# Optimization experiments

Measured on AMD Instinct MI355X. Metric: run time of the kernel, lower is better.

The kernel has to match this reference:

```python
import jax, jax.numpy as jnp
import numpy as np

N_NODES = 100000
N_EDGES = 800000
ANNOT = 92
HID = 64
N_STEPS = 8
N_IDX = 20000


def setup_inputs() -> dict:
    key = jax.random.key(0)
    ks = jax.random.split(key, 12)
    s = 1.0 / np.sqrt(HID)
    return {
        'x': jax.random.normal(ks[0], (N_NODES, ANNOT), dtype=jnp.float32),
        'edge_index': jax.random.randint(ks[1], (2, N_EDGES), 0, N_NODES, dtype=jnp.int64),
        'idx': jax.random.randint(ks[2], (N_IDX,), 0, N_NODES, dtype=jnp.int64),
        'W_red': jax.random.normal(ks[3], (ANNOT, HID), dtype=jnp.float32) / np.sqrt(ANNOT),
        'b_red': jnp.zeros((HID,), dtype=jnp.float32),
        'W_g': jax.random.normal(ks[4], (N_STEPS, HID, HID), dtype=jnp.float32) * s,
        'w_ih': jax.random.normal(ks[5], (3 * HID, HID), dtype=jnp.float32) * s,
        'w_hh': jax.random.normal(ks[6], (3 * HID, HID), dtype=jnp.float32) * s,
        'b_ih': jax.random.normal(ks[7], (3 * HID,), dtype=jnp.float32) * s,
        'b_hh': jax.random.normal(ks[8], (3 * HID,), dtype=jnp.float32) * s,
        'W_lin': jax.random.normal(ks[9], (HID, 1), dtype=jnp.float32) * s,
        'b_lin': jnp.zeros((1,), dtype=jnp.float32),
    }


def _gru_cell(a, h, w_ih, w_hh, b_ih, b_hh):
    # a: aggregated messages [N, H]; h: hidden state [N, H]
    gi = a @ w_ih.T + b_ih  # [N, 3H]
    gh = h @ w_hh.T + b_hh
    i_r, i_z, i_n = jnp.split(gi, 3, axis=-1)
    h_r, h_z, h_n = jnp.split(gh, 3, axis=-1)
    r = jax.nn.sigmoid(i_r + h_r)
    z = jax.nn.sigmoid(i_z + h_z)
    n = jnp.tanh(i_n + r * h_n)
    return (1.0 - z) * n + z * h


def reference(x, edge_index, idx, W_red, b_red, W_g, w_ih, w_hh, b_ih, b_hh, W_lin, b_lin):
    src, dst = edge_index[0], edge_index[1]
    h = x @ W_red + b_red  # [N, H]

    def step(h, Wt):
        m = h @ Wt                                  # [N, H] per-step transform
        msg = jnp.take(m, src, axis=0)              # gather along edges [E, H]
        aggr = jax.ops.segment_sum(msg, dst, num_segments=N_NODES)  # scatter-add
        h_new = _gru_cell(aggr, h, w_ih, w_hh, b_ih, b_hh)
        return h_new, None

    h, _ = jax.lax.scan(step, h, W_g)
    sel = jnp.take(h, idx, axis=0)                  # index_select [B, H]
    return jax.nn.sigmoid(sel @ W_lin + b_lin)      # [B, 1]
```

## Files before the change

### kernel.cpp

```cpp
#include <hip/hip_runtime.h>
#include <hip/hip_bf16.h>

#define NN 100000
#define HH 64
#define AN 92
#define NSTEP 8
#define NGRP 6250
#define RB 768
#define CAP 64

typedef float f4v __attribute__((ext_vector_type(4)));
typedef short s8v __attribute__((ext_vector_type(8)));

__device__ __forceinline__ float sigf(float x) { return 1.0f / (1.0f + __expf(-x)); }
__device__ __forceinline__ float tanhfast(float x) { return 1.0f - 2.0f / (1.0f + __expf(2.0f * x)); }

__device__ __forceinline__ unsigned short tobf(float x) {
    __hip_bfloat16 b = __float2bfloat16(x);
    return __builtin_bit_cast(unsigned short, b);
}
__device__ __forceinline__ float frombf(unsigned short u) {
    return __int_as_float(((unsigned)u) << 16);
}

__device__ __forceinline__ int packpos(int k, int r) {
    int T = r >> 4, kh = k >> 5;
    int lane = ((k >> 3) & 3) * 16 + (r & 15);
    int j = k & 7;
    return ((T * 2 + kh) * 64 + lane) * 8 + j;
}

__global__ __launch_bounds__(256) void k_wcp(const float* __restrict__ Wg,
                                             const float* __restrict__ w_ih,
                                             const float* __restrict__ w_hh,
                                             unsigned short* __restrict__ Wcp,
                                             unsigned short* __restrict__ Whp) {
    __shared__ float wl[192 * 65];
    int wb = blockIdx.x;
    if (wb < 384) {
        for (int i = threadIdx.x; i < 192 * 64; i += 256) {
            int r = i >> 6, q = i & 63;
            wl[r * 65 + q] = w_ih[i];
        }
        __syncthreads();
        int gid = wb * 256 + threadIdx.x;
        int r = gid % 192;
        int k = (gid / 192) & 63;
        int t = gid / (192 * 64);
        const float* wg = Wg + t * 4096 + k * 64;
        float acc = 0.f;
#pragma unroll
        for (int q = 0; q < 64; ++q) acc = fmaf(wg[q], wl[r * 65 + q], acc);
        Wcp[t * 12288 + packpos(k, r)] = tobf(acc);
    } else {
        int gid = (wb - 384) * 256 + threadIdx.x;
        if (gid >= 192 * 64) return;
        int r = gid >> 6, k = gid & 63;
        Whp[packpos(k, r)] = tobf(w_hh[r * 64 + k]);
    }
}

__global__ __launch_bounds__(256) void k_plred(const int* __restrict__ src,
                                               const int* __restrict__ dst,
                                               int* __restrict__ cnt,
                                               int* __restrict__ srt, int E,
                                               const float* __restrict__ x,
                                               const float* __restrict__ W,
                                               const float* __restrict__ b,
                                               unsigned short* __restrict__ hb) {
    __shared__ float xl[16][96];
    __shared__ float wl[96 * 64];
    int tid = threadIdx.x;
    if (blockIdx.x >= RB) {
        int e = (blockIdx.x - RB) * 256 + tid;
        if (e < E) {
            int d = dst[e];
            int pos = atomicAdd(cnt + d, 1);
            if (pos < CAP) srt[d * CAP + pos] = src[e];
        }
        return;
    }
    for (int i = tid; i < AN * 64; i += 256) wl[i] = W[i];
    wl[AN * 64 + tid] = 0.f;
    if (tid < 64) xl[tid >> 2][AN + (tid & 3)] = 0.f;
    int lane = tid & 63, wave = tid >> 6;
    float bj = b[lane];

    for (int g = blockIdx.x; g < NGRP; g += RB) {
        int n0 = g * 16;
        __syncthreads();
        for (int i = tid; i < 16 * AN; i += 256)
            xl[i / AN][i % AN] = x[(size_t)n0 * AN + i];
        __syncthreads();
        float a[4];
#pragma unroll
        for (int u = 0; u < 4; ++u) a[u] = bj;
#pragma unroll
        for (int k4 = 0; k4 < 96; k4 += 4) {
            float4 xv[4];
#pragma unroll
            for (int u = 0; u < 4; ++u) xv[u] = *(const float4*)&xl[wave * 4 + u][k4];
#pragma unroll
            for (int kk = 0; kk < 4; ++kk) {
                float wv = wl[(k4 + kk) * 64 + lane];
                a[0] = fmaf(((const float*)&xv[0])[kk], wv, a[0]);
                a[1] = fmaf(((const float*)&xv[1])[kk], wv, a[1]);
                a[2] = fmaf(((const float*)&xv[2])[kk], wv, a[2]);
                a[3] = fmaf(((const float*)&xv[3])[kk], wv, a[3]);
            }
        }
#pragma unroll
        for (int u = 0; u < 4; ++u) {
            int n = n0 + wave * 4 + u;
            hb[(size_t)n * HH + lane] = tobf(a[u]);
        }
    }
}

__global__ __launch_bounds__(256) void k_aggr(const unsigned short* __restrict__ hb,
                                              const int* __restrict__ cnt,
                                              const int* __restrict__ srt,
                                              unsigned short* __restrict__ Sb) {
    int gid = blockIdx.x * 256 + threadIdx.x;
    int wid = gid >> 6;
    int lane = threadIdx.x & 63;
    int half = lane >> 5;
    int ci = lane & 31;
    int n = wid * 2 + half;
    if (n >= NN) return;
    int st = n * CAP;
    int en = st + min(cnt[n], CAP);
    float aa[8], bb[8];
#pragma unroll
    for (int i = 0; i < 8; ++i) { aa[i] = 0.f; bb[i] = 0.f; }
    for (int j = st; j < en; j += 8) {
        unsigned u[8];
#pragma unroll
        for (int i = 0; i < 8; ++i) {
            int jj = j + i;
            int sidx = srt[min(jj, en - 1)];
            unsigned uu = *(const unsigned*)(hb + (size_t)sidx * HH + ci * 2);
            u[i] = (jj < en) ? uu : 0u;
        }
#pragma unroll
        for (int i = 0; i < 8; ++i) {
            aa[i] += frombf((unsigned short)u[i]);
            bb[i] += frombf((unsigned short)(u[i] >> 16));
        }
    }
    float A = ((aa[0] + aa[1]) + (aa[2] + aa[3])) + ((aa[4] + aa[5]) + (aa[6] + aa[7]));
    float B = ((bb[0] + bb[1]) + (bb[2] + bb[3])) + ((bb[4] + bb[5]) + (bb[6] + bb[7]));
    unsigned o = (unsigned)tobf(A) | ((unsigned)tobf(B) << 16);
    *(unsigned*)(Sb + (size_t)n * HH + ci * 2) = o;
}

__global__ __launch_bounds__(256) void k_gru(const unsigned short* __restrict__ Sb,
                                             unsigned short* __restrict__ hb,
                                             const unsigned short* __restrict__ Wcp_t,
                                             const unsigned short* __restrict__ Whp,
                                             const float* __restrict__ b_ih,
                                             const float* __restrict__ b_hh) {
    const s8v* wiB = (const s8v*)Wcp_t;
    const s8v* whB = (const s8v*)Whp;

    int lane = threadIdx.x & 63;
    int wave = threadIdx.x >> 6;
    int quad = lane >> 4, nidx = lane & 15;
    int g = blockIdx.x * 4 + wave;
    if (g >= NGRP) return;

    float brz[4], bzz[4], bin[4], bhn[4];
#pragma unroll
    for (int t = 0; t < 4; ++t) {
        int c = t * 16 + nidx;
        brz[t] = b_ih[c] + b_hh[c];
        bzz[t] = b_ih[64 + c] + b_hh[64 + c];
        bin[t] = b_ih[128 + c];
        bhn[t] = b_hh[128 + c];
    }

    int n0 = g * 16;
    size_t rowoff = (size_t)(n0 + nidx) * HH + quad * 8;
    s8v aS0 = *(const s8v*)(Sb + rowoff);
    s8v aS1 = *(const s8v*)(Sb + rowoff + 32);
    s8v aH0 = *(const s8v*)(hb + rowoff);
    s8v aH1 = *(const s8v*)(hb + rowoff + 32);

#pragma unroll
    for (int t = 0; t < 4; ++t) {
        f4v aRZ0 = {brz[t], brz[t], brz[t], brz[t]};
        f4v aRZ1 = {bzz[t], bzz[t], bzz[t], bzz[t]};
        f4v aIN  = {bin[t], bin[t], bin[t], bin[t]};
        f4v aHN  = {bhn[t], bhn[t], bhn[t], bhn[t]};
        aRZ0 = __builtin_amdgcn_mfma_f32_16x16x32_bf16(aS0, wiB[(t * 2 + 0) * 64 + lane], aRZ0, 0, 0, 0);
        aRZ0 = __builtin_amdgcn_mfma_f32_16x16x32_bf16(aS1, wiB[(t * 2 + 1) * 64 + lane], aRZ0, 0, 0, 0);
        aRZ0 = __builtin_amdgcn_mfma_f32_16x16x32_bf16(aH0, whB[(t * 2 + 0) * 64 + lane], aRZ0, 0, 0, 0);
        aRZ0 = __builtin_amdgcn_mfma_f32_16x16x32_bf16(aH1, whB[(t * 2 + 1) * 64 + lane], aRZ0, 0, 0, 0);
        int tz = t + 4;
        aRZ1 = __builtin_amdgcn_mfma_f32_16x16x32_bf16(aS0, wiB[(tz * 2 + 0) * 64 + lane], aRZ1, 0, 0, 0);
        aRZ1 = __builtin_amdgcn_mfma_f32_16x16x32_bf16(aS1, wiB[(tz * 2 + 1) * 64 + lane], aRZ1, 0, 0, 0);
        aRZ1 = __builtin_amdgcn_mfma_f32_16x16x32_bf16(aH0, whB[(tz * 2 + 0) * 64 + lane], aRZ1, 0, 0, 0);
        aRZ1 = __builtin_amdgcn_mfma_f32_16x16x32_bf16(aH1, whB[(tz * 2 + 1) * 64 + lane], aRZ1, 0, 0, 0);
        int tn = t + 8;
        aIN = __builtin_amdgcn_mfma_f32_16x16x32_bf16(aS0, wiB[(tn * 2 + 0) * 64 + lane], aIN, 0, 0, 0);
        aIN = __builtin_amdgcn_mfma_f32_16x16x32_bf16(aS1, wiB[(tn * 2 + 1) * 64 + lane], aIN, 0, 0, 0);
        aHN = __builtin_amdgcn_mfma_f32_16x16x32_bf16(aH0, whB[(tn * 2 + 0) * 64 + lane], aHN, 0, 0, 0);
        aHN = __builtin_amdgcn_mfma_f32_16x16x32_bf16(aH1, whB[(tn * 2 + 1) * 64 + lane], aHN, 0, 0, 0);
        int c = t * 16 + nidx;
#pragma unroll
        for (int reg = 0; reg < 4; ++reg) {
            int node = n0 + quad * 4 + reg;
            float rv = sigf(aRZ0[reg]);
            float zv = sigf(aRZ1[reg]);
            float nv = tanhfast(fmaf(rv, aHN[reg], aIN[reg]));
            size_t off = (size_t)node * HH + c;
            float ho = frombf(hb[off]);
            float hnew = fmaf(zv, ho - nv, nv);
            hb[off] = tobf(hnew);
        }
    }
}

__global__ __launch_bounds__(256) void k_readout(const unsigned short* __restrict__ hb,
                                                 const int* __restrict__ idx,
                                                 const float* __restrict__ Wl,
                                                 const float* __restrict__ bl,
                                                 float* __restrict__ out, int B) {
    int gid = blockIdx.x * 256 + threadIdx.x;
    int i = gid >> 6, lane = gid & 63;
    if (i >= B) return;
    int n = idx[i];
    float v = frombf(hb[(size_t)n * HH + lane]) * Wl[lane];
#pragma unroll
    for (int off = 32; off > 0; off >>= 1) v += __shfl_xor(v, off, 64);
    if (lane == 0) out[i] = sigf(v + bl[0]);
}

extern "C" void kernel_launch(void* const* d_in, const int* in_sizes, int n_in,
                              void* d_out, int out_size, void* d_ws, size_t ws_size,
                              hipStream_t stream) {
    const float* x     = (const float*)d_in[0];
    const int*   ei    = (const int*)d_in[1];
    const int*   idx   = (const int*)d_in[2];
    const float* W_red = (const float*)d_in[3];
    const float* b_red = (const float*)d_in[4];
    const float* W_g   = (const float*)d_in[5];
    const float* w_ih  = (const float*)d_in[6];
    const float* w_hh  = (const float*)d_in[7];
    const float* b_ih  = (const float*)d_in[8];
    const float* b_hh  = (const float*)d_in[9];
    const float* W_lin = (const float*)d_in[10];
    const float* b_lin = (const float*)d_in[11];
    float* out = (float*)d_out;
    const int E = in_sizes[1] / 2;
    const int B = in_sizes[2];
    const int* src = ei;
    const int* dst = ei + E;
    const int PB = (E + 255) / 256;

    unsigned short* hb  = (unsigned short*)d_ws;
    unsigned short* Sb  = hb + (size_t)NN * HH;
    unsigned short* Wcp = Sb + (size_t)NN * HH;
    unsigned short* Whp = Wcp + (size_t)NSTEP * 12288;
    int*            cnt = (int*)(Whp + 12288);
    int*            srt = cnt + NN;

    hipMemsetAsync(cnt, 0, NN * sizeof(int), stream);
    k_wcp<<<384 + 48, 256, 0, stream>>>(W_g, w_ih, w_hh, Wcp, Whp);

    k_plred<<<RB + PB, 256, 0, stream>>>(src, dst, cnt, srt, E,
                                         x, W_red, b_red, hb);

    for (int t = 0; t < NSTEP; ++t) {
        k_aggr<<<(NN / 2 * 64 + 255) / 256, 256, 0, stream>>>(hb, cnt, srt, Sb);
        k_gru<<<1563, 256, 0, stream>>>(Sb, hb, Wcp + (size_t)t * 12288, Whp,
                                        b_ih, b_hh);
    }

    k_readout<<<(B * 64 + 255) / 256, 256, 0, stream>>>(hb, idx, W_lin, b_lin, out, B);
}
```

Baseline: 528.4 us.

## Use bf16 MFMA for input reduction and fuse weight prep into plred launch

Rewrites the x@W_red projection to use 16x16x32 bf16 MFMA, with W_red packed into shared memory and each wave handling a 16-node group. The separate weight-combination kernel is merged into the same launch as extra blocks, which saves one launch and its serialization. Inputs x are rounded to bf16 before the matmul, which adds a small precision loss compared with the fp32 FMA path. The w_ih shared-memory staging is dropped in favour of direct global reads.

Measured after the change: 527.0 us. Within noise of the previous version (-0.3%).

```diff
diff --git a/kernel.cpp b/kernel.cpp
--- a/kernel.cpp
+++ b/kernel.cpp
@@ -7,6 +7,7 @@
 #define NSTEP 8
 #define NGRP 6250
 #define RB 768
+#define WCB 432
 #define CAP 64
 
 typedef float f4v __attribute__((ext_vector_type(4)));
@@ -28,36 +29,6 @@
     int lane = ((k >> 3) & 3) * 16 + (r & 15);
     int j = k & 7;
     return ((T * 2 + kh) * 64 + lane) * 8 + j;
-}
-
-__global__ __launch_bounds__(256) void k_wcp(const float* __restrict__ Wg,
-                                             const float* __restrict__ w_ih,
-                                             const float* __restrict__ w_hh,
-                                             unsigned short* __restrict__ Wcp,
-                                             unsigned short* __restrict__ Whp) {
-    __shared__ float wl[192 * 65];
-    int wb = blockIdx.x;
-    if (wb < 384) {
-        for (int i = threadIdx.x; i < 192 * 64; i += 256) {
-            int r = i >> 6, q = i & 63;
-            wl[r * 65 + q] = w_ih[i];
-        }
-        __syncthreads();
-        int gid = wb * 256 + threadIdx.x;
-        int r = gid % 192;
-        int k = (gid / 192) & 63;
-        int t = gid / (192 * 64);
-        const float* wg = Wg + t * 4096 + k * 64;
-        float acc = 0.f;
-#pragma unroll
-        for (int q = 0; q < 64; ++q) acc = fmaf(wg[q], wl[r * 65 + q], acc);
-        Wcp[t * 12288 + packpos(k, r)] = tobf(acc);
-    } else {
-        int gid = (wb - 384) * 256 + threadIdx.x;
-        if (gid >= 192 * 64) return;
-        int r = gid >> 6, k = gid & 63;
-        Whp[packpos(k, r)] = tobf(w_hh[r * 64 + k]);
-    }
 }
 
 __global__ __launch_bounds__(256) void k_plred(const int* __restrict__ src,
@@ -67,12 +38,38 @@
                                                const float* __restrict__ x,
                                                const float* __restrict__ W,
                                                const float* __restrict__ b,
-                                               unsigned short* __restrict__ hb) {
-    __shared__ float xl[16][96];
-    __shared__ float wl[96 * 64];
+                                               unsigned short* __restrict__ hb,
+                                               const float* __restrict__ Wg,
+                                               const float* __restrict__ w_ih,
+                                               const float* __restrict__ w_hh,
+                                               unsigned short* __restrict__ Wcp,
+                                               unsigned short* __restrict__ Whp) {
+    __shared__ __align__(16) unsigned short wrp[6144];
     int tid = threadIdx.x;
     if (blockIdx.x >= RB) {
-        int e = (blockIdx.x - RB) * 256 + tid;
+        int wb = blockIdx.x - RB;
+        if (wb < WCB) {
+            if (wb < 384) {
+                int gid = wb * 256 + tid;
+                int r = gid % 192;
+                int k = (gid / 192) & 63;
+                int t = gid / (192 * 64);
+                const float* wg = Wg + t * 4096 + k * 64;
+                const float* wi = w_ih + r * 64;
+                float acc = 0.f;
+#pragma unroll
+                for (int q = 0; q < 64; ++q) acc = fmaf(wg[q], wi[q], acc);
+                Wcp[t * 12288 + packpos(k, r)] = tobf(acc);
+            } else {
+                int gid = (wb - 384) * 256 + tid;
+                if (gid < 192 * 64) {
+                    int r = gid >> 6, k = gid & 63;
+                    Whp[packpos(k, r)] = tobf(w_hh[r * 64 + k]);
+                }
+            }
+            return;
+        }
+        int e = (wb - WCB) * 256 + tid;
         if (e < E) {
             int d = dst[e];
             int pos = atomicAdd(cnt + d, 1);
@@ -80,39 +77,51 @@
         }
         return;
     }
-    for (int i = tid; i < AN * 64; i += 256) wl[i] = W[i];
-    wl[AN * 64 + tid] = 0.f;
-    if (tid < 64) xl[tid >> 2][AN + (tid & 3)] = 0.f;
+    for (int i = tid; i < 96 * 64; i += 256) {
+        int k = i >> 6, r = i & 63;
+        float val = (k < AN) ? W[k * HH + r] : 0.f;
+        int T = r >> 4, kh = k >> 5;
+        int ln = ((k >> 3) & 3) * 16 + (r & 15);
+        int j = k & 7;
+        wrp[((T * 3 + kh) * 64 + ln) * 8 + j] = tobf(val);
+    }
+    __syncthreads();
+    const s8v* wB = (const s8v*)wrp;
     int lane = tid & 63, wave = tid >> 6;
-    float bj = b[lane];
-
-    for (int g = blockIdx.x; g < NGRP; g += RB) {
+    int row16 = lane & 15, quad = lane >> 4;
+    float bj[4];
+#pragma unroll
+    for (int t = 0; t < 4; ++t) bj[t] = b[t * 16 + row16];
+
+    for (int g = blockIdx.x * 4 + wave; g < NGRP; g += RB * 4) {
         int n0 = g * 16;
-        __syncthreads();
-        for (int i = tid; i < 16 * AN; i += 256)
-            xl[i / AN][i % AN] = x[(size_t)n0 * AN + i];
-        __syncthreads();
-        float a[4];
-#pragma unroll
-        for (int u = 0; u < 4; ++u) a[u] = bj;
-#pragma unroll
-        for (int k4 = 0; k4 < 96; k4 += 4) {
-            float4 xv[4];
-#pragma unroll
-            for (int u = 0; u < 4; ++u) xv[u] = *(const float4*)&xl[wave * 4 + u][k4];
-#pragma unroll
-            for (int kk = 0; kk < 4; ++kk) {
-                float wv = wl[(k4 + kk) * 64 + lane];
-                a[0] = fmaf(((const float*)&xv[0])[kk], wv, a[0]);
-                a[1] = fmaf(((const float*)&xv[1])[kk], wv, a[1]);
-                a[2] = fmaf(((const float*)&xv[2])[kk], wv, a[2]);
-                a[3] = fmaf(((const float*)&xv[3])[kk], wv, a[3]);
+        const float* xp = x + (size_t)(n0 + row16) * AN;
+        s8v A[3];
+#pragma unroll
+        for (int kh = 0; kh < 3; ++kh) {
+            int k0 = quad * 8 + kh * 32;
+            float4 lo = *(const float4*)(xp + k0);
+            float4 hi;
+            if (kh == 2 && quad == 3) hi = make_float4(0.f, 0.f, 0.f, 0.f);
+            else hi = *(const float4*)(xp + k0 + 4);
+            s8v f;
+            f[0] = (short)tobf(lo.x); f[1] = (short)tobf(lo.y);
+            f[2] = (short)tobf(lo.z); f[3] = (short)tobf(lo.w);
+            f[4] = (short)tobf(hi.x); f[5] = (short)tobf(hi.y);
+            f[6] = (short)tobf(hi.z); f[7] = (short)tobf(hi.w);
+            A[kh] = f;
+        }
+#pragma unroll
+        for (int t = 0; t < 4; ++t) {
+            f4v acc = {bj[t], bj[t], bj[t], bj[t]};
+#pragma unroll
+            for (int kh = 0; kh < 3; ++kh)
+                acc = __builtin_amdgcn_mfma_f32_16x16x32_bf16(A[kh], wB[(t * 3 + kh) * 64 + lane], acc, 0, 0, 0);
+#pragma unroll
+            for (int reg = 0; reg < 4; ++reg) {
+                int node = n0 + quad * 4 + reg;
+                hb[(size_t)node * HH + t * 16 + row16] = tobf(acc[reg]);
             }
-        }
-#pragma unroll
-        for (int u = 0; u < 4; ++u) {
-            int n = n0 + wave * 4 + u;
-            hb[(size_t)n * HH + lane] = tobf(a[u]);
         }
     }
 }
@@ -266,10 +275,9 @@
     int*            srt = cnt + NN;
 
     hipMemsetAsync(cnt, 0, NN * sizeof(int), stream);
-    k_wcp<<<384 + 48, 256, 0, stream>>>(W_g, w_ih, w_hh, Wcp, Whp);
-
-    k_plred<<<RB + PB, 256, 0, stream>>>(src, dst, cnt, srt, E,
-                                         x, W_red, b_red, hb);
+    k_plred<<<RB + WCB + PB, 256, 0, stream>>>(src, dst, cnt, srt, E,
+                                               x, W_red, b_red, hb,
+                                               W_g, w_ih, w_hh, Wcp, Whp);
 
     for (int t = 0; t < NSTEP; ++t) {
         k_aggr<<<(NN / 2 * 64 + 255) / 256, 256, 0, stream>>>(hb, cnt, srt, Sb);
```
